# Performance work log

Hardware: AMD Instinct MI355X
Metric: run time of the kernel (lower is better)

## Reference

```python
import jax, jax.numpy as jnp
import numpy as np

N_NODES = 100_000
N_EDGES = 1_600_000
C_IN = 256
C_OUT = 128


def setup_inputs() -> dict:
    key = jax.random.key(0)
    k_x, k_e, k_w = jax.random.split(key, 3)
    x = jax.random.normal(k_x, (N_NODES, C_IN), dtype=jnp.float32)
    edge_index = jax.random.randint(k_e, (2, N_EDGES), 0, N_NODES, dtype=jnp.int64)
    # GCNConv linear weight (glorot-ish scale) and bias
    W = jax.random.normal(k_w, (C_IN, C_OUT), dtype=jnp.float32) * (1.0 / np.sqrt(C_IN))
    b = jnp.zeros((C_OUT,), dtype=jnp.float32)
    # PReLU per-channel slope, torch default init 0.25
    alpha = jnp.full((C_OUT,), 0.25, dtype=jnp.float32)
    return {"x": x, "edge_index": edge_index, "W": W, "b": b, "alpha": alpha}


def reference(x, edge_index, W, b, alpha):
    N = x.shape[0]
    # GCNConv: add self-loops
    loop = jnp.arange(N, dtype=edge_index.dtype)
    src = jnp.concatenate([edge_index[0], loop])  # message sources (row)
    dst = jnp.concatenate([edge_index[1], loop])  # aggregation targets (col)
    # symmetric normalization: deg computed at targets with unit edge weights
    ones = jnp.ones(src.shape[0], dtype=x.dtype)
    deg = jax.ops.segment_sum(ones, dst, num_segments=N)
    deg_inv_sqrt = jnp.where(deg > 0, jax.lax.rsqrt(deg), 0.0)
    norm = deg_inv_sqrt[src] * deg_inv_sqrt[dst]  # [E+N]
    # linear transform then normalized scatter-add aggregation
    xw = x @ W  # [N, C_OUT]
    msg = xw[src] * norm[:, None]  # [E+N, C_OUT] gathered messages
    out = jax.ops.segment_sum(msg, dst, num_segments=N) + b  # [N, C_OUT]
    # per-channel PReLU
    return jnp.where(out > 0, out, alpha * out)
```

## Files before the change

kernel.cpp:

```cpp
#include <hip/hip_runtime.h>

#define CIN 256
#define COUT 128
#define BSH2 9
#define BN2 512
#define NBA 256
#define TILE_E 8192

typedef __attribute__((ext_vector_type(8))) short short8;
typedef __attribute__((ext_vector_type(4))) float f32x4;

__device__ __forceinline__ unsigned f2bf(float x) {
    unsigned u = __float_as_uint(x);
    unsigned r = ((u >> 16) & 1u) + 0x7fffu;
    return (u + r) >> 16;
}
__device__ __forceinline__ float bflo(unsigned u) { return __uint_as_float(u << 16); }
__device__ __forceinline__ float bfhi(unsigned u) { return __uint_as_float(u & 0xffff0000u); }


__global__ __launch_bounds__(256) void k_hist1(const int* __restrict__ dst,
                                               int* __restrict__ histT, int e, int nt) {
    __shared__ int h[NBA];
    const int tid = threadIdx.x;
    const int t = blockIdx.x;
    h[tid] = 0;
    __syncthreads();
    const int lo = t * TILE_E;
    const int hi = min(lo + TILE_E, e);
    for (int i = lo + tid; i < hi; i += 256)
        atomicAdd(&h[dst[i] >> BSH2], 1);
    __syncthreads();
    histT[tid * nt + t] = h[tid];
}

__global__ __launch_bounds__(256) void k_scanA(const int* __restrict__ histT,
                                               int* __restrict__ baseT,
                                               int* __restrict__ tot, int nt) {
    __shared__ int v[256];
    const int b = blockIdx.x;
    const int tid = threadIdx.x;
    int carry = 0;
    for (int c0 = 0; c0 < nt; c0 += 256) {
        int t = c0 + tid;
        int x = (t < nt) ? histT[b * nt + t] : 0;
        v[tid] = x;
        __syncthreads();
        for (int off = 1; off < 256; off <<= 1) {
            int add = (tid >= off) ? v[tid - off] : 0;
            __syncthreads();
            v[tid] += add;
            __syncthreads();
        }
        if (t < nt) baseT[b * nt + t] = carry + v[tid] - x;
        carry += v[255];
        __syncthreads();
    }
    if (tid == 0) tot[b] = carry;
}

__global__ __launch_bounds__(256) void k_scanB(const int* __restrict__ tot,
                                               int* __restrict__ bbase, int e) {
    __shared__ int v[256];
    const int tid = threadIdx.x;
    int x = tot[tid];
    v[tid] = x;
    __syncthreads();
    for (int off = 1; off < 256; off <<= 1) {
        int add = (tid >= off) ? v[tid - off] : 0;
        __syncthreads();
        v[tid] += add;
        __syncthreads();
    }
    bbase[tid] = v[tid] - x;
    if (tid == 0) bbase[NBA] = e;
}

__global__ __launch_bounds__(256) void k_scatter1(const int* __restrict__ src,
                                                  const int* __restrict__ dst,
                                                  const int* __restrict__ baseT,
                                                  const int* __restrict__ bbase,
                                                  int* __restrict__ etmp, int e, int nt) {
    __shared__ int cur[NBA];
    const int tid = threadIdx.x;
    const int t = blockIdx.x;
    cur[tid] = bbase[tid] + baseT[tid * nt + t];
    __syncthreads();
    const int lo = t * TILE_E;
    const int hi = min(lo + TILE_E, e);
    for (int i = lo + tid; i < hi; i += 256) {
        int d = dst[i];
        int p = atomicAdd(&cur[d >> BSH2], 1);
        etmp[p] = ((d & (BN2 - 1)) << 17) | src[i];
    }
}


__global__ __launch_bounds__(256) void k_bbuild_a(const int* __restrict__ etmp,
                                                  const int* __restrict__ bbase,
                                                  int* __restrict__ ecnt,
                                                  float* __restrict__ dinv,
                                                  int* __restrict__ offset, int n) {
    __shared__ int h[BN2];
    __shared__ int val[256];
    __shared__ int sc[BN2];
    const int b = blockIdx.x;
    const int tid = threadIdx.x;
    const int base = bbase[b];
    const int cnt = bbase[b + 1] - base;

    h[tid] = 0; h[tid + 256] = 0;
    __syncthreads();
    for (int i = tid; i < cnt; i += 256)
        atomicAdd(&h[etmp[base + i] >> 17], 1);
    __syncthreads();
    val[tid] = h[2 * tid] + h[2 * tid + 1];
    __syncthreads();
    for (int off = 1; off < 256; off <<= 1) {
        int add = (tid >= off) ? val[tid - off] : 0;
        __syncthreads();
        val[tid] += add;
        __syncthreads();
    }
    int excl = (tid == 0) ? 0 : val[tid - 1];
    sc[2 * tid] = excl;
    sc[2 * tid + 1] = excl + h[2 * tid];
    __syncthreads();
#pragma unroll
    for (int q = 0; q < 2; q++) {
        int nd = 2 * tid + q;
        int v = (b << BSH2) + nd;
        if (v < n) {
            ecnt[v] = h[nd];
            dinv[v] = rsqrtf((float)(h[nd] + 1));
            offset[v] = base + sc[nd];
        }
    }
}


__global__ __launch_bounds__(256) void k_bbuild_b(const int* __restrict__ etmp,
                                                  const int* __restrict__ bbase,
                                                  const int* __restrict__ offset,
                                                  int* __restrict__ src_csr, int n) {
    __shared__ int sc[BN2];
    __shared__ int cur[BN2];
    const int b = blockIdx.x;
    const int tid = threadIdx.x;
    const int base = bbase[b];
    const int cnt = bbase[b + 1] - base;

#pragma unroll
    for (int q = 0; q < 2; q++) {
        int nd = 2 * tid + q;
        int v = (b << BSH2) + nd;
        sc[nd] = (v < n) ? (offset[v] - base) : 0;
        cur[nd] = 0;
    }
    __syncthreads();
    for (int i = tid; i < cnt; i += 256) {
        int pk = etmp[base + i];
        int dl = pk >> 17;
        int p = atomicAdd(&cur[dl], 1);
        src_csr[base + sc[dl] + p] = pk & 0x1FFFF;
    }
}


__global__ __launch_bounds__(256) void k_packW(const float* __restrict__ W,
                                               uint4* __restrict__ Wp) {
    int t = blockIdx.x * 256 + threadIdx.x;
    int lane = t & 63;
    int nt = (t >> 6) & 7;
    int kt = t >> 9;
    int kbase = kt * 32 + (lane >> 4) * 8;
    int col = nt * 16 + (lane & 15);
    unsigned o[4];
#pragma unroll
    for (int jj = 0; jj < 4; jj++) {
        float a = W[(size_t)(kbase + 2 * jj) * COUT + col];
        float b = W[(size_t)(kbase + 2 * jj + 1) * COUT + col];
        o[jj] = f2bf(a) | (f2bf(b) << 16);
    }
    Wp[t] = make_uint4(o[0], o[1], o[2], o[3]);
}


__global__ __launch_bounds__(256) void k_gemm_mfma(const float* __restrict__ X,
                                                   const uint4* __restrict__ Wp,
                                                   const float* __restrict__ dinv,
                                                   unsigned short* __restrict__ XWb, int n) {
    const int wave = threadIdx.x >> 6;
    const int lane = threadIdx.x & 63;
    const int row0 = blockIdx.x * 64 + wave * 16;
    int arow = row0 + (lane & 15);
    if (arow >= n) arow = n - 1;
    const int kgrp = (lane >> 4) * 8;

    f32x4 acc[8];
#pragma unroll
    for (int i = 0; i < 8; i++) acc[i] = (f32x4)0.f;

    const float* xptr = X + (size_t)arow * CIN + kgrp;

    union U { unsigned u[4]; short8 s; };

#pragma unroll
    for (int kt = 0; kt < 8; kt++) {
        float4 a0 = *(const float4*)(xptr + kt * 32);
        float4 a1 = *(const float4*)(xptr + kt * 32 + 4);
        U au;
        au.u[0] = f2bf(a0.x) | (f2bf(a0.y) << 16);
        au.u[1] = f2bf(a0.z) | (f2bf(a0.w) << 16);
        au.u[2] = f2bf(a1.x) | (f2bf(a1.y) << 16);
        au.u[3] = f2bf(a1.z) | (f2bf(a1.w) << 16);
        short8 afrag = au.s;
#pragma unroll
        for (int nt = 0; nt < 8; nt++) {
            uint4 b = Wp[(kt * 8 + nt) * 64 + lane];
            U bu;
            bu.u[0] = b.x; bu.u[1] = b.y; bu.u[2] = b.z; bu.u[3] = b.w;
            acc[nt] = __builtin_amdgcn_mfma_f32_16x16x32_bf16(afrag, bu.s, acc[nt], 0, 0, 0);
        }
    }

    const int r0 = (lane >> 4) * 4;
    const int c = lane & 15;
#pragma unroll
    for (int r = 0; r < 4; r++) {
        int row = row0 + r0 + r;
        if (row < n) {
            float dv = dinv[row];
#pragma unroll
            for (int nt = 0; nt < 8; nt++)
                XWb[(size_t)row * COUT + nt * 16 + c] = (unsigned short)f2bf(dv * acc[nt][r]);
        }
    }
}


__global__ __launch_bounds__(256) void k_agg(const unsigned* __restrict__ XWb,
                                             const float* __restrict__ dinv,
                                             const int* __restrict__ ecnt,
                                             const int* __restrict__ offset,
                                             const int* __restrict__ src_csr,
                                             const float* __restrict__ bias,
                                             const float* __restrict__ alpha,
                                             float* __restrict__ out, int n) {
    const int wave = threadIdx.x >> 6;
    const int lane = threadIdx.x & 63;
    const int v = blockIdx.x * 4 + wave;
    if (v >= n) return;

    const float dv = dinv[v];
    float ax, ay;
    {
        unsigned u = XWb[(size_t)v * 64 + lane];
        ax = bflo(u);
        ay = bfhi(u);
    }
    const int beg = offset[v];
    const int cnt = ecnt[v];
    int e = 0;
    for (; e + 8 <= cnt; e += 8) {
        int s[8];
#pragma unroll
        for (int q = 0; q < 8; q++) s[q] = src_csr[beg + e + q];
        unsigned u[8];
#pragma unroll
        for (int q = 0; q < 8; q++) u[q] = XWb[(size_t)s[q] * 64 + lane];
#pragma unroll
        for (int q = 0; q < 8; q++) {
            ax += bflo(u[q]);
            ay += bfhi(u[q]);
        }
    }
    for (; e + 4 <= cnt; e += 4) {
        int s[4];
#pragma unroll
        for (int q = 0; q < 4; q++) s[q] = src_csr[beg + e + q];
        unsigned u[4];
#pragma unroll
        for (int q = 0; q < 4; q++) u[q] = XWb[(size_t)s[q] * 64 + lane];
#pragma unroll
        for (int q = 0; q < 4; q++) {
            ax += bflo(u[q]);
            ay += bfhi(u[q]);
        }
    }
    for (; e < cnt; e++) {
        int s = src_csr[beg + e];
        unsigned u = XWb[(size_t)s * 64 + lane];
        ax += bflo(u);
        ay += bfhi(u);
    }
    float2 bb = *(const float2*)&bias[lane * 2];
    float2 aa = *(const float2*)&alpha[lane * 2];
    float o0 = dv * ax + bb.x;
    float o1 = dv * ay + bb.y;
    o0 = o0 > 0.f ? o0 : aa.x * o0;
    o1 = o1 > 0.f ? o1 : aa.y * o1;
    *(float2*)&out[(size_t)v * COUT + lane * 2] = make_float2(o0, o1);
}


extern "C" void kernel_launch(void* const* d_in, const int* in_sizes, int n_in,
                              void* d_out, int out_size, void* d_ws, size_t ws_size,
                              hipStream_t stream) {
    const float* x     = (const float*)d_in[0];
    const int*   edge  = (const int*)d_in[1];
    const float* W     = (const float*)d_in[2];
    const float* bias  = (const float*)d_in[3];
    const float* alpha = (const float*)d_in[4];
    float* out = (float*)d_out;

    const int n = in_sizes[0] / CIN;
    const int e = in_sizes[1] / 2;
    const int* src = edge;
    const int* dst = edge + e;
    const int nt  = (e + TILE_E - 1) / TILE_E;
    const int nb1 = (n + BN2 - 1) >> BSH2;

    char* ws = (char*)d_ws;
    unsigned* xwb   = (unsigned*)ws;
    char* p = ws + (size_t)n * (COUT / 2) * 4;
    float* dinv     = (float*)p;            p += (size_t)n * 4;
    int*   ecnt     = (int*)p;              p += (size_t)n * 4;
    int*   offset   = (int*)p;              p += (size_t)n * 4;
    int*   src_csr  = (int*)p;              p += (size_t)e * 4;
    int*   etmp     = (int*)p;              p += (size_t)e * 4;
    uint4* wpack    = (uint4*)p;            p += 4096 * 16;
    int*   histT    = (int*)p;              p += (size_t)NBA * nt * 4;
    int*   baseT    = (int*)p;              p += (size_t)NBA * nt * 4;
    int*   bbase    = (int*)p;              p += (size_t)(NBA + 1) * 4;
    int*   tot      = (int*)p;              p += (size_t)NBA * 4;

    const int TB = 256;
    k_hist1<<<nt, TB, 0, stream>>>(dst, histT, e, nt);
    k_scanA<<<NBA, TB, 0, stream>>>(histT, baseT, tot, nt);
    k_scanB<<<1, TB, 0, stream>>>(tot, bbase, e);
    k_scatter1<<<nt, TB, 0, stream>>>(src, dst, baseT, bbase, etmp, e, nt);
    k_bbuild_a<<<nb1, TB, 0, stream>>>(etmp, bbase, ecnt, dinv, offset, n);
    k_bbuild_b<<<nb1, TB, 0, stream>>>(etmp, bbase, offset, src_csr, n);
    k_packW<<<16, TB, 0, stream>>>(W, wpack);
    k_gemm_mfma<<<(n + 63) / 64, TB, 0, stream>>>(x, wpack, dinv, (unsigned short*)xwb, n);
    k_agg<<<(n + 3) / 4, TB, 0, stream>>>(xwb, dinv, ecnt, offset, src_csr, bias, alpha, out, n);
}
```

Baseline: 164.6 us.

## Fuse setup kernels, pack bf16 XW rows as channel pairs, unroll aggregation by 16

Folds the W packing into the histogram kernel as extra blocks and merges the two bucket-build kernels into one, cutting two launches and a re-read of offsets. The GEMM epilogue now writes packed 32-bit words holding channels c and c+64, so each lane's aggregation load matches its output channels and the final store becomes two coalesced scalar writes. The aggregation loop gains a 16-edge unrolled stage to keep more gathers in flight, which raises register pressure.

```diff
diff --git a/kernel.cpp b/kernel.cpp
--- a/kernel.cpp
+++ b/kernel.cpp
@@ -19,10 +19,29 @@
 __device__ __forceinline__ float bfhi(unsigned u) { return __uint_as_float(u & 0xffff0000u); }
 
 
-__global__ __launch_bounds__(256) void k_hist1(const int* __restrict__ dst,
-                                               int* __restrict__ histT, int e, int nt) {
+__global__ __launch_bounds__(256) void k_histpack(const int* __restrict__ dst,
+                                                  int* __restrict__ histT,
+                                                  const float* __restrict__ W,
+                                                  uint4* __restrict__ Wp, int e, int nt) {
+    const int tid = threadIdx.x;
+    if ((int)blockIdx.x >= nt) {
+        int t = (blockIdx.x - nt) * 256 + tid;
+        int lane = t & 63;
+        int ntile = (t >> 6) & 7;
+        int kt = t >> 9;
+        int kbase = kt * 32 + (lane >> 4) * 8;
+        int col = ntile * 16 + (lane & 15);
+        unsigned o[4];
+#pragma unroll
+        for (int jj = 0; jj < 4; jj++) {
+            float a = W[(size_t)(kbase + 2 * jj) * COUT + col];
+            float b = W[(size_t)(kbase + 2 * jj + 1) * COUT + col];
+            o[jj] = f2bf(a) | (f2bf(b) << 16);
+        }
+        Wp[t] = make_uint4(o[0], o[1], o[2], o[3]);
+        return;
+    }
     __shared__ int h[NBA];
-    const int tid = threadIdx.x;
     const int t = blockIdx.x;
     h[tid] = 0;
     __syncthreads();
@@ -96,14 +115,16 @@
 }
 
 
-__global__ __launch_bounds__(256) void k_bbuild_a(const int* __restrict__ etmp,
-                                                  const int* __restrict__ bbase,
-                                                  int* __restrict__ ecnt,
-                                                  float* __restrict__ dinv,
-                                                  int* __restrict__ offset, int n) {
+__global__ __launch_bounds__(256) void k_bbuild(const int* __restrict__ etmp,
+                                                const int* __restrict__ bbase,
+                                                int* __restrict__ ecnt,
+                                                float* __restrict__ dinv,
+                                                int* __restrict__ offset,
+                                                int* __restrict__ src_csr, int n) {
     __shared__ int h[BN2];
     __shared__ int val[256];
     __shared__ int sc[BN2];
+    __shared__ int cur[BN2];
     const int b = blockIdx.x;
     const int tid = threadIdx.x;
     const int base = bbase[b];
@@ -130,32 +151,12 @@
     for (int q = 0; q < 2; q++) {
         int nd = 2 * tid + q;
         int v = (b << BSH2) + nd;
+        cur[nd] = 0;
         if (v < n) {
             ecnt[v] = h[nd];
             dinv[v] = rsqrtf((float)(h[nd] + 1));
             offset[v] = base + sc[nd];
         }
-    }
-}
-
-
-__global__ __launch_bounds__(256) void k_bbuild_b(const int* __restrict__ etmp,
-                                                  const int* __restrict__ bbase,
-                                                  const int* __restrict__ offset,
-                                                  int* __restrict__ src_csr, int n) {
-    __shared__ int sc[BN2];
-    __shared__ int cur[BN2];
-    const int b = blockIdx.x;
-    const int tid = threadIdx.x;
-    const int base = bbase[b];
-    const int cnt = bbase[b + 1] - base;
-
-#pragma unroll
-    for (int q = 0; q < 2; q++) {
-        int nd = 2 * tid + q;
-        int v = (b << BSH2) + nd;
-        sc[nd] = (v < n) ? (offset[v] - base) : 0;
-        cur[nd] = 0;
     }
     __syncthreads();
     for (int i = tid; i < cnt; i += 256) {
@@ -167,29 +168,10 @@
 }
 
 
-__global__ __launch_bounds__(256) void k_packW(const float* __restrict__ W,
-                                               uint4* __restrict__ Wp) {
-    int t = blockIdx.x * 256 + threadIdx.x;
-    int lane = t & 63;
-    int nt = (t >> 6) & 7;
-    int kt = t >> 9;
-    int kbase = kt * 32 + (lane >> 4) * 8;
-    int col = nt * 16 + (lane & 15);
-    unsigned o[4];
-#pragma unroll
-    for (int jj = 0; jj < 4; jj++) {
-        float a = W[(size_t)(kbase + 2 * jj) * COUT + col];
-        float b = W[(size_t)(kbase + 2 * jj + 1) * COUT + col];
-        o[jj] = f2bf(a) | (f2bf(b) << 16);
-    }
-    Wp[t] = make_uint4(o[0], o[1], o[2], o[3]);
-}
-
-
 __global__ __launch_bounds__(256) void k_gemm_mfma(const float* __restrict__ X,
                                                    const uint4* __restrict__ Wp,
                                                    const float* __restrict__ dinv,
-                                                   unsigned short* __restrict__ XWb, int n) {
+                                                   unsigned* __restrict__ XWb, int n) {
     const int wave = threadIdx.x >> 6;
     const int lane = threadIdx.x & 63;
     const int row0 = blockIdx.x * 64 + wave * 16;
@@ -232,8 +214,11 @@
         if (row < n) {
             float dv = dinv[row];
 #pragma unroll
-            for (int nt = 0; nt < 8; nt++)
-                XWb[(size_t)row * COUT + nt * 16 + c] = (unsigned short)f2bf(dv * acc[nt][r]);
+            for (int k = 0; k < 4; k++) {
+                unsigned wlo = f2bf(dv * acc[k][r]);
+                unsigned whi = f2bf(dv * acc[k + 4][r]);
+                XWb[(size_t)row * 64 + c + 16 * k] = wlo | (whi << 16);
+            }
         }
     }
 }
@@ -262,6 +247,19 @@
     const int beg = offset[v];
     const int cnt = ecnt[v];
     int e = 0;
+    for (; e + 16 <= cnt; e += 16) {
+        int s[16];
+#pragma unroll
+        for (int q = 0; q < 16; q++) s[q] = src_csr[beg + e + q];
+        unsigned u[16];
+#pragma unroll
+        for (int q = 0; q < 16; q++) u[q] = XWb[(size_t)s[q] * 64 + lane];
+#pragma unroll
+        for (int q = 0; q < 16; q++) {
+            ax += bflo(u[q]);
+            ay += bfhi(u[q]);
+        }
+    }
     for (; e + 8 <= cnt; e += 8) {
         int s[8];
 #pragma unroll
@@ -294,13 +292,14 @@
         ax += bflo(u);
         ay += bfhi(u);
     }
-    float2 bb = *(const float2*)&bias[lane * 2];
-    float2 aa = *(const float2*)&alpha[lane * 2];
-    float o0 = dv * ax + bb.x;
-    float o1 = dv * ay + bb.y;
-    o0 = o0 > 0.f ? o0 : aa.x * o0;
-    o1 = o1 > 0.f ? o1 : aa.y * o1;
-    *(float2*)&out[(size_t)v * COUT + lane * 2] = make_float2(o0, o1);
+    float blo = bias[lane],  bhi = bias[lane + 64];
+    float alo = alpha[lane], ahi = alpha[lane + 64];
+    float o0 = dv * ax + blo;
+    float o1 = dv * ay + bhi;
+    o0 = o0 > 0.f ? o0 : alo * o0;
+    o1 = o1 > 0.f ? o1 : ahi * o1;
+    out[(size_t)v * COUT + lane] = o0;
+    out[(size_t)v * COUT + lane + 64] = o1;
 }
 
 
@@ -336,13 +335,11 @@
     int*   tot      = (int*)p;              p += (size_t)NBA * 4;
 
     const int TB = 256;
-    k_hist1<<<nt, TB, 0, stream>>>(dst, histT, e, nt);
+    k_histpack<<<nt + 16, TB, 0, stream>>>(dst, histT, W, wpack, e, nt);
     k_scanA<<<NBA, TB, 0, stream>>>(histT, baseT, tot, nt);
     k_scanB<<<1, TB, 0, stream>>>(tot, bbase, e);
     k_scatter1<<<nt, TB, 0, stream>>>(src, dst, baseT, bbase, etmp, e, nt);
-    k_bbuild_a<<<nb1, TB, 0, stream>>>(etmp, bbase, ecnt, dinv, offset, n);
-    k_bbuild_b<<<nb1, TB, 0, stream>>>(etmp, bbase, offset, src_csr, n);
-    k_packW<<<16, TB, 0, stream>>>(W, wpack);
-    k_gemm_mfma<<<(n + 63) / 64, TB, 0, stream>>>(x, wpack, dinv, (unsigned short*)xwb, n);
+    k_bbuild<<<nb1, TB, 0, stream>>>(etmp, bbase, ecnt, dinv, offset, src_csr, n);
+    k_gemm_mfma<<<(n + 63) / 64, TB, 0, stream>>>(x, wpack, dinv, xwb, n);
     k_agg<<<(n + 3) / 4, TB, 0, stream>>>(xwb, dinv, ecnt, offset, src_csr, bias, alpha, out, n);
 }
```

New measurement: 157.9 us. -4.1%, faster.
